# Kernel optimization log

Hardware: AMD Instinct MI355X
Metric: run time of the kernel (lower is better)

Reference implementation:

```python
import jax, jax.numpy as jnp
import numpy as np

B, A, D, F, O, NB = 64, 1024, 5, 256, 256, 6  # batch, max_atoms, max_degree, ishape, oshape, bond feat dim


def setup_inputs() -> dict:
    key = jax.random.key(0)
    k1, k2, k3, k4 = jax.random.split(key, 4)
    atoms = jax.random.normal(k1, (B, A, F), dtype=jnp.float32)
    bonds = jax.random.normal(k2, (B, A, D, NB), dtype=jnp.float32)
    # -1 marks missing neighbor (degree padding); valid indices in [0, A)
    edges = jax.random.randint(k3, (B, A, D), -1, A)
    # xavier-normal-ish init for the 6 degree-specific weights, stacked [6, F+NB, O]
    scale = (2.0 / (F + NB + O)) ** 0.5
    degW = jax.random.normal(k4, (6, F + NB, O), dtype=jnp.float32) * scale
    b = jnp.full((1, O), 0.01, dtype=jnp.float32)
    return {"atoms": atoms, "bonds": bonds, "edges": edges, "degW": degW, "b": b}


def reference(atoms, bonds, edges, degW, b):
    # atoms: [B, A, F]; bonds: [B, A, D, NB]; edges: [B, A, D] int (-1 = pad)
    degrees = (edges != -1).sum(-1, keepdims=True)  # [B, A, 1]
    # pad a zero row at index 0 so edge -1 -> 0 gathers the mask value 0
    padded = jnp.pad(atoms, ((0, 0), (1, 0), (0, 0)))  # [B, A+1, F]
    neigh = jax.vmap(lambda p, e: p[e])(padded, edges + 1)  # [B, A, D, F]
    summed_atom = atoms + neigh.sum(axis=2)  # include_self=True
    feats = jnp.concatenate([summed_atom, bonds.sum(axis=2)], axis=-1)  # [B, A, F+NB]
    out = jnp.zeros((atoms.shape[0], atoms.shape[1], degW.shape[-1]), atoms.dtype)
    for d in range(6):  # fixed small structural loop over degree buckets
        mask = (degrees == d).astype(atoms.dtype)  # [B, A, 1]
        out = out + jax.nn.sigmoid(feats @ degW[d] + b) * mask
    return out
```

## Files before the change

### kernel.cpp

```cpp
#include <hip/hip_runtime.h>
#include <cstdint>

#define BATCH  64
#define NATOMS 1024
#define DEG    5
#define FIN    256
#define OOUT   256
#define NBF    6
#define KDIM   262
#define KP     288
#define NKT    9
#define MROWS  (BATCH * NATOMS)
#define MT     32
#define AS     296

typedef __attribute__((ext_vector_type(8))) short bf16x8;
typedef __attribute__((ext_vector_type(4))) float f32x4;

__device__ __forceinline__ unsigned short f2bf(float x) {
    unsigned u = __float_as_uint(x);
    u += 0x7fff + ((u >> 16) & 1);
    return (unsigned short)(u >> 16);
}
__device__ __forceinline__ float bf2f(unsigned short h) {
    return __uint_as_float(((unsigned)h) << 16);
}
__device__ __forceinline__ float sigmoidf_(float x) {
    return 1.f / (1.f + __expf(-x));
}

__global__ __launch_bounds__(256)
void convert_w_kernel(const float* __restrict__ degW, unsigned short* __restrict__ Wsw)
{
    const int idx = blockIdx.x * 256 + threadIdx.x;
    if (idx >= 16 * NKT * 64) return;
    const int lane = idx & 63;
    const int t    = (idx >> 6) % NKT;
    const int g    = (idx >> 6) / NKT;
    const int col  = g * 16 + (lane & 15);
    const int k0   = t * 32 + (lane >> 4) * 8;
    const float* __restrict__ W5 = degW + (size_t)DEG * KDIM * OOUT;
    unsigned short* dst = Wsw + (size_t)idx * 8;
    #pragma unroll
    for (int j = 0; j < 8; ++j) {
        const int k = k0 + j;
        dst[j] = f2bf((k < KDIM) ? W5[(size_t)k * OOUT + col] : 0.f);
    }
}

__global__ __launch_bounds__(256, 4)
void nfp_fused_kernel(const float* __restrict__ atoms, const float* __restrict__ bonds,
                      const int* __restrict__ edges, const unsigned short* __restrict__ Wsw,
                      const float* __restrict__ degW, const float* __restrict__ bias,
                      float* __restrict__ out)
{
    __shared__ short Afeat[MT * AS];
    __shared__ int   edg[MT * DEG];
    __shared__ int   deg_lds[MT];

    const int tid  = threadIdx.x;
    const int lane = tid & 63;
    const int wave = tid >> 6;

    const int bid   = blockIdx.x;
    const int xcd   = bid & 7;
    const int per   = bid >> 3;
    const int batch = (per >> 5) * 8 + xcd;
    const int blk   = per & 31;
    const int row0  = batch * NATOMS + blk * MT;

    if (tid < MT * DEG) edg[tid] = edges[row0 * DEG + tid];
    __syncthreads();
    if (tid < MT) {
        int dc = 0;
        #pragma unroll
        for (int d = 0; d < DEG; ++d) dc += (edg[tid * DEG + d] != -1) ? 1 : 0;
        deg_lds[tid] = dc;
    }

    const float* __restrict__ abase = atoms + ((size_t)batch << 10) * FIN;
    #pragma unroll 2
    for (int mi = 0; mi < 8; ++mi) {
        const int m = wave * 8 + mi;
        int   ei[DEG];
        float fl[DEG];
        #pragma unroll
        for (int d = 0; d < DEG; ++d) {
            const int e = edg[m * DEG + d];
            ei[d] = (e >= 0) ? e : 0;
            fl[d] = (e >= 0) ? 1.f : 0.f;
        }
        float4 v = *(const float4*)&atoms[((size_t)row0 + m) * FIN + lane * 4];
        float4 nv[DEG];
        #pragma unroll
        for (int d = 0; d < DEG; ++d)
            nv[d] = *(const float4*)&abase[(size_t)ei[d] * FIN + lane * 4];
        #pragma unroll
        for (int d = 0; d < DEG; ++d) {
            v.x += fl[d] * nv[d].x; v.y += fl[d] * nv[d].y;
            v.z += fl[d] * nv[d].z; v.w += fl[d] * nv[d].w;
        }
        ushort4 us;
        us.x = f2bf(v.x); us.y = f2bf(v.y); us.z = f2bf(v.z); us.w = f2bf(v.w);
        *(ushort4*)&Afeat[m * AS + lane * 4] = us;
        if (lane < 32) {
            float bv = 0.f;
            if (lane < NBF) {
                const float* bb = bonds + ((size_t)row0 + m) * (DEG * NBF);
                #pragma unroll
                for (int d = 0; d < DEG; ++d) bv += bb[d * NBF + lane];
            }
            Afeat[m * AS + FIN + lane] = f2bf(bv);
        }
    }
    __syncthreads();

    const int fr = lane & 15;
    const int q  = lane >> 4;
    const int wn = wave * 64;

    f32x4 acc[2][4];
    #pragma unroll
    for (int i = 0; i < 2; ++i)
        #pragma unroll
        for (int j = 0; j < 4; ++j)
            acc[i][j] = (f32x4){0.f, 0.f, 0.f, 0.f};

    #pragma unroll
    for (int t = 0; t < NKT; ++t) {
        bf16x8 af[2], bfr[4];
        #pragma unroll
        for (int i = 0; i < 2; ++i)
            af[i] = *(const bf16x8*)&Afeat[(i * 16 + fr) * AS + t * 32 + q * 8];
        #pragma unroll
        for (int j = 0; j < 4; ++j)
            bfr[j] = *(const bf16x8*)&Wsw[((size_t)((wave * 4 + j) * NKT + t) * 64 + lane) * 8];
        #pragma unroll
        for (int i = 0; i < 2; ++i)
            #pragma unroll
            for (int j = 0; j < 4; ++j)
                acc[i][j] = __builtin_amdgcn_mfma_f32_16x16x32_bf16(af[i], bfr[j], acc[i][j], 0, 0, 0);
    }

    #pragma unroll
    for (int j = 0; j < 4; ++j) {
        const int gn = wn + j * 16 + fr;
        const float bj = bias[gn];
        #pragma unroll
        for (int i = 0; i < 2; ++i) {
            #pragma unroll
            for (int r = 0; r < 4; ++r) {
                const int lm = i * 16 + q * 4 + r;
                if (deg_lds[lm] == DEG)
                    out[((size_t)row0 + lm) * OOUT + gn] = sigmoidf_(acc[i][j][r] + bj);
            }
        }
    }

    for (int m = 0; m < MT; ++m) {
        const int d = deg_lds[m];
        if (d == DEG) continue;
        const float* __restrict__ W = degW + (size_t)d * KDIM * OOUT;
        float a2 = 0.f;
        #pragma unroll 2
        for (int k = 0; k < KDIM; ++k)
            a2 += bf2f(Afeat[m * AS + k]) * W[(size_t)k * OOUT + tid];
        out[((size_t)row0 + m) * OOUT + tid] = sigmoidf_(a2 + bias[tid]);
    }
}

#define FMT  32
#define FKT  32
#define FKPAD 288
__global__ __launch_bounds__(256, 2)
void nfp_conv_fallback(const float* __restrict__ atoms, const float* __restrict__ bonds,
                       const int* __restrict__ edges, const float* __restrict__ degW,
                       const float* __restrict__ bias, float* __restrict__ out)
{
    __shared__ float feats[FMT * FKPAD];
    __shared__ float wtile[FKT * OOUT];
    __shared__ int   edg[FMT * DEG];
    __shared__ int   deg_lds[FMT];
    __shared__ int   odd_list[FMT];
    __shared__ int   odd_cnt;
    __shared__ float b_lds[OOUT];

    const int tid = threadIdx.x, bid = blockIdx.x;
    const int batch = bid >> 5, a0 = (bid & 31) * FMT;
    const size_t atom_base = (size_t)batch * NATOMS;

    b_lds[tid] = bias[tid];
    if (tid == 0) odd_cnt = 0;
    if (tid < FMT * DEG) {
        const int m = tid / DEG, d = tid % DEG;
        edg[tid] = edges[(atom_base + a0 + m) * DEG + d];
    }
    __syncthreads();
    if (tid < FMT) {
        int dc = 0;
        #pragma unroll
        for (int d = 0; d < DEG; ++d) dc += (edg[tid * DEG + d] != -1) ? 1 : 0;
        deg_lds[tid] = dc;
        if (dc != DEG) { const int idx = atomicAdd(&odd_cnt, 1); odd_list[idx] = tid; }
    }
    __syncthreads();
    {
        const int f = tid;
        for (int m = 0; m < FMT; ++m) {
            float v = atoms[(atom_base + a0 + m) * FIN + f];
            #pragma unroll
            for (int d = 0; d < DEG; ++d) {
                const int e = edg[m * DEG + d];
                if (e >= 0) v += atoms[(atom_base + e) * FIN + f];
            }
            feats[m * FKPAD + f] = v;
        }
        #pragma unroll
        for (int t = 0; t < 4; ++t) {
            const int idx = t * 256 + tid;
            const int m = idx >> 5, kk = idx & 31;
            float v = 0.f;
            if (kk < NBF) {
                const size_t bb = (atom_base + a0 + m) * (size_t)(DEG * NBF);
                #pragma unroll
                for (int d = 0; d < DEG; ++d) v += bonds[bb + d * NBF + kk];
            }
            feats[m * FKPAD + FIN + kk] = v;
        }
    }
    const float* __restrict__ W5 = degW + (size_t)DEG * KDIM * OOUT;
    float acc[4][8];
    #pragma unroll
    for (int i = 0; i < 4; ++i)
        #pragma unroll
        for (int j = 0; j < 8; ++j) acc[i][j] = 0.f;
    const int tx = tid & 31, ty = tid >> 5;
    for (int kt = 0; kt < FKPAD; kt += FKT) {
        __syncthreads();
        #pragma unroll
        for (int t = 0; t < FKT; ++t) {
            const int k = kt + t;
            wtile[t * OOUT + tid] = (k < KDIM) ? W5[(size_t)k * OOUT + tid] : 0.f;
        }
        __syncthreads();
        #pragma unroll 4
        for (int r = 0; r < FKT; ++r) {
            float a_frag[4];
            #pragma unroll
            for (int i = 0; i < 4; ++i) a_frag[i] = feats[(ty * 4 + i) * FKPAD + kt + r];
            float w_frag[8];
            #pragma unroll
            for (int j = 0; j < 8; ++j) w_frag[j] = wtile[r * OOUT + tx + j * 32];
            #pragma unroll
            for (int i = 0; i < 4; ++i)
                #pragma unroll
                for (int j = 0; j < 8; ++j) acc[i][j] += a_frag[i] * w_frag[j];
        }
    }
    #pragma unroll
    for (int i = 0; i < 4; ++i) {
        const int m = ty * 4 + i;
        if (deg_lds[m] == DEG) {
            const size_t row = (atom_base + a0 + m) * (size_t)OOUT;
            #pragma unroll
            for (int j = 0; j < 8; ++j) {
                const int o = tx + j * 32;
                out[row + o] = sigmoidf_(acc[i][j] + b_lds[o]);
            }
        }
    }
    const int ocnt = odd_cnt;
    for (int i = 0; i < ocnt; ++i) {
        const int m = odd_list[i], d = deg_lds[m];
        const float* __restrict__ W = degW + (size_t)d * KDIM * OOUT;
        float a2 = 0.f;
        for (int k = 0; k < KDIM; ++k) a2 += feats[m * FKPAD + k] * W[(size_t)k * OOUT + tid];
        const size_t row = (atom_base + a0 + m) * (size_t)OOUT;
        out[row + tid] = sigmoidf_(a2 + b_lds[tid]);
    }
}

extern "C" void kernel_launch(void* const* d_in, const int* in_sizes, int n_in,
                              void* d_out, int out_size, void* d_ws, size_t ws_size,
                              hipStream_t stream) {
    const float* atoms = (const float*)d_in[0];
    const float* bonds = (const float*)d_in[1];
    const int*   edges = (const int*)d_in[2];
    const float* degW  = (const float*)d_in[3];
    const float* bias  = (const float*)d_in[4];
    float* out = (float*)d_out;

    const size_t WSW_BYTES = (size_t)16 * NKT * 64 * 8 * 2;

    if (ws_size < WSW_BYTES) {
        nfp_conv_fallback<<<BATCH * (NATOMS / FMT), 256, 0, stream>>>(
            atoms, bonds, edges, degW, bias, out);
        return;
    }

    unsigned short* Wsw = (unsigned short*)d_ws;
    convert_w_kernel<<<(16 * NKT * 64 + 255) / 256, 256, 0, stream>>>(degW, Wsw);
    nfp_fused_kernel<<<MROWS / MT, 256, 0, stream>>>(
        atoms, bonds, edges, Wsw, degW, bias, out);
}
```

Before: 228.2 us.

## Batch neighbor gathers, prefetch weight fragments, split accumulators in fallback rows

The gather phase now issues loads for two rows' self and neighbor vectors before accumulating, and spreads the bond-sum work across all lanes. This is meant to raise memory-level parallelism and hide gather latency. The MFMA loop double-buffers the B fragments so the next k-tile's weights load while the current MFMAs run. Full-degree output uses nontemporal stores, and the scalar path for rows with other degrees uses four independent accumulators to break the dependency chain. The cost is higher register pressure, which may reduce occupancy.

```diff
diff --git a/kernel.cpp b/kernel.cpp
--- a/kernel.cpp
+++ b/kernel.cpp
@@ -79,39 +79,48 @@
     }
 
     const float* __restrict__ abase = atoms + ((size_t)batch << 10) * FIN;
-    #pragma unroll 2
-    for (int mi = 0; mi < 8; ++mi) {
-        const int m = wave * 8 + mi;
-        int   ei[DEG];
-        float fl[DEG];
-        #pragma unroll
-        for (int d = 0; d < DEG; ++d) {
-            const int e = edg[m * DEG + d];
-            ei[d] = (e >= 0) ? e : 0;
-            fl[d] = (e >= 0) ? 1.f : 0.f;
-        }
-        float4 v = *(const float4*)&atoms[((size_t)row0 + m) * FIN + lane * 4];
-        float4 nv[DEG];
-        #pragma unroll
-        for (int d = 0; d < DEG; ++d)
-            nv[d] = *(const float4*)&abase[(size_t)ei[d] * FIN + lane * 4];
-        #pragma unroll
-        for (int d = 0; d < DEG; ++d) {
-            v.x += fl[d] * nv[d].x; v.y += fl[d] * nv[d].y;
-            v.z += fl[d] * nv[d].z; v.w += fl[d] * nv[d].w;
-        }
-        ushort4 us;
-        us.x = f2bf(v.x); us.y = f2bf(v.y); us.z = f2bf(v.z); us.w = f2bf(v.w);
-        *(ushort4*)&Afeat[m * AS + lane * 4] = us;
-        if (lane < 32) {
-            float bv = 0.f;
-            if (lane < NBF) {
-                const float* bb = bonds + ((size_t)row0 + m) * (DEG * NBF);
-                #pragma unroll
-                for (int d = 0; d < DEG; ++d) bv += bb[d * NBF + lane];
-            }
-            Afeat[m * AS + FIN + lane] = f2bf(bv);
-        }
+    const int selfrow = blk * MT;
+    #pragma unroll
+    for (int c = 0; c < 4; ++c) {
+        const int mb = wave * 8 + c * 2;
+        float4 self[2];
+        float4 nv[2][DEG];
+        #pragma unroll
+        for (int r = 0; r < 2; ++r) {
+            const int m = mb + r;
+            self[r] = *(const float4*)&abase[(size_t)(selfrow + m) * FIN + lane * 4];
+            #pragma unroll
+            for (int d = 0; d < DEG; ++d) {
+                const int e  = edg[m * DEG + d];
+                const int ei = (e >= 0) ? e : 0;
+                nv[r][d] = *(const float4*)&abase[(size_t)ei * FIN + lane * 4];
+            }
+        }
+        #pragma unroll
+        for (int r = 0; r < 2; ++r) {
+            const int m = mb + r;
+            float4 v = self[r];
+            #pragma unroll
+            for (int d = 0; d < DEG; ++d) {
+                const float fl = (edg[m * DEG + d] >= 0) ? 1.f : 0.f;
+                v.x += fl * nv[r][d].x; v.y += fl * nv[r][d].y;
+                v.z += fl * nv[r][d].z; v.w += fl * nv[r][d].w;
+            }
+            ushort4 us;
+            us.x = f2bf(v.x); us.y = f2bf(v.y); us.z = f2bf(v.z); us.w = f2bf(v.w);
+            *(ushort4*)&Afeat[m * AS + lane * 4] = us;
+        }
+    }
+    #pragma unroll
+    for (int i = lane; i < 8 * 32; i += 64) {
+        const int r  = i >> 5, kk = i & 31;
+        const int m  = wave * 8 + r;
+        float bv = 0.f;
+        if (kk < NBF) {
+            const float* bb = bonds + ((size_t)row0 + m) * (DEG * NBF) + kk;
+            bv = bb[0] + bb[NBF] + bb[2 * NBF] + bb[3 * NBF] + bb[4 * NBF];
+        }
+        Afeat[m * AS + FIN + kk] = f2bf(bv);
     }
     __syncthreads();
 
@@ -126,20 +135,29 @@
         for (int j = 0; j < 4; ++j)
             acc[i][j] = (f32x4){0.f, 0.f, 0.f, 0.f};
 
+    bf16x8 bcur[4], bnxt[4];
+    #pragma unroll
+    for (int j = 0; j < 4; ++j)
+        bcur[j] = *(const bf16x8*)&Wsw[((size_t)((wave * 4 + j) * NKT) * 64 + lane) * 8];
+
     #pragma unroll
     for (int t = 0; t < NKT; ++t) {
-        bf16x8 af[2], bfr[4];
+        if (t + 1 < NKT) {
+            #pragma unroll
+            for (int j = 0; j < 4; ++j)
+                bnxt[j] = *(const bf16x8*)&Wsw[((size_t)((wave * 4 + j) * NKT + t + 1) * 64 + lane) * 8];
+        }
+        bf16x8 af[2];
         #pragma unroll
         for (int i = 0; i < 2; ++i)
             af[i] = *(const bf16x8*)&Afeat[(i * 16 + fr) * AS + t * 32 + q * 8];
         #pragma unroll
-        for (int j = 0; j < 4; ++j)
-            bfr[j] = *(const bf16x8*)&Wsw[((size_t)((wave * 4 + j) * NKT + t) * 64 + lane) * 8];
-        #pragma unroll
         for (int i = 0; i < 2; ++i)
             #pragma unroll
             for (int j = 0; j < 4; ++j)
-                acc[i][j] = __builtin_amdgcn_mfma_f32_16x16x32_bf16(af[i], bfr[j], acc[i][j], 0, 0, 0);
+                acc[i][j] = __builtin_amdgcn_mfma_f32_16x16x32_bf16(af[i], bcur[j], acc[i][j], 0, 0, 0);
+        #pragma unroll
+        for (int j = 0; j < 4; ++j) bcur[j] = bnxt[j];
     }
 
     #pragma unroll
@@ -152,20 +170,32 @@
             for (int r = 0; r < 4; ++r) {
                 const int lm = i * 16 + q * 4 + r;
                 if (deg_lds[lm] == DEG)
-                    out[((size_t)row0 + lm) * OOUT + gn] = sigmoidf_(acc[i][j][r] + bj);
+                    __builtin_nontemporal_store(sigmoidf_(acc[i][j][r] + bj),
+                                                &out[((size_t)row0 + lm) * OOUT + gn]);
             }
         }
     }
 
     for (int m = 0; m < MT; ++m) {
-        const int d = deg_lds[m];
-        if (d == DEG) continue;
-        const float* __restrict__ W = degW + (size_t)d * KDIM * OOUT;
-        float a2 = 0.f;
+        const int dg = deg_lds[m];
+        if (dg == DEG) continue;
+        const float* __restrict__ W = degW + (size_t)dg * KDIM * OOUT;
+        float s0 = 0.f, s1 = 0.f, s2 = 0.f, s3 = 0.f;
         #pragma unroll 2
-        for (int k = 0; k < KDIM; ++k)
-            a2 += bf2f(Afeat[m * AS + k]) * W[(size_t)k * OOUT + tid];
-        out[((size_t)row0 + m) * OOUT + tid] = sigmoidf_(a2 + bias[tid]);
+        for (int k = 0; k < 260; k += 4) {
+            const float w0 = W[(size_t)(k + 0) * OOUT + tid];
+            const float w1 = W[(size_t)(k + 1) * OOUT + tid];
+            const float w2 = W[(size_t)(k + 2) * OOUT + tid];
+            const float w3 = W[(size_t)(k + 3) * OOUT + tid];
+            s0 += bf2f(Afeat[m * AS + k + 0]) * w0;
+            s1 += bf2f(Afeat[m * AS + k + 1]) * w1;
+            s2 += bf2f(Afeat[m * AS + k + 2]) * w2;
+            s3 += bf2f(Afeat[m * AS + k + 3]) * w3;
+        }
+        s0 += bf2f(Afeat[m * AS + 260]) * W[(size_t)260 * OOUT + tid];
+        s1 += bf2f(Afeat[m * AS + 261]) * W[(size_t)261 * OOUT + tid];
+        const float x = ((s0 + s1) + (s2 + s3)) + bias[tid];
+        out[((size_t)row0 + m) * OOUT + tid] = sigmoidf_(x);
     }
 }
 
```

Result: faster. 198.3 us (-13.1%).
